# Kernel tuning notes

Measured on AMD Instinct MI355X. Metric: run time of the kernel, lower is better.

Reference implementation:

```python
import jax, jax.numpy as jnp
import numpy as np

EPS = 1e-5  # torch BatchNorm default eps
B, C, T, NOUT, NCLS = 4096, 32, 512, 16, 4


def setup_inputs() -> dict:
    key = jax.random.key(0)
    ks = jax.random.split(key, 12)
    s = lambda k, shape: jax.random.normal(k, shape, jnp.float32) * 0.05
    return {
        "de": jax.random.normal(ks[0], (B, C, T), jnp.float32),
        "adj": jax.random.normal(ks[1], (B, C, C), jnp.float32),  # unused by forward (module recomputes corr)
        "dw_w": s(ks[2], (C, 1, 3)),      # depthwise Conv1d weight [C,1,3]
        "dw_b": s(ks[3], (C,)),
        "pw_w": s(ks[4], (C, C)),          # pointwise 1x1 conv [out,in]
        "pw_b": s(ks[5], (C,)),
        "bn1_g": jnp.ones((C,), jnp.float32),
        "bn1_b": jnp.zeros((C,), jnp.float32),
        "gc_w": s(ks[6], (T, NOUT)),       # GraphConvolution weight
        "fc_w": s(ks[7], (C * NOUT, C)),   # fc62 Linear(512,32)
        "fc_b": s(ks[8], (C,)),
        "bn2_g": jnp.ones((C,), jnp.float32),
        "bn2_b": jnp.zeros((C,), jnp.float32),
        "cls_w": s(ks[9], (C, NCLS)),      # fcclass Linear(32,4)
        "cls_b": s(ks[10], (NCLS,)),
    }


def reference(de, adj, dw_w, dw_b, pw_w, pw_b, bn1_g, bn1_b, gc_w,
              fc_w, fc_b, bn2_g, bn2_b, cls_w, cls_b):
    # --- SeparableConv2d (really 1d): depthwise k=3 -> pointwise 1x1 -> BN -> relu ---
    x = jax.lax.conv_general_dilated(
        de, dw_w, window_strides=(1,), padding=[(1, 1)],
        dimension_numbers=("NCH", "OIH", "NCH"),
        feature_group_count=de.shape[1]) + dw_b[None, :, None]
    x = jnp.einsum("oc,bct->bot", pw_w, x) + pw_b[None, :, None]
    m = x.mean((0, 2), keepdims=True)
    v = x.var((0, 2), keepdims=True)  # biased, as BN normalization uses
    x = (x - m) / jnp.sqrt(v + EPS) * bn1_g[None, :, None] + bn1_b[None, :, None]
    x = jax.nn.relu(x)                       # [B, C, T]

    # --- batched Pearson corrcoef over the time axis (vectorizes the per-sample loop) ---
    xt = x.transpose(0, 2, 1)                # [B, T, C]
    Tn = xt.shape[1]
    f = (Tn - 1) / Tn
    xc = xt - xt.mean(1, keepdims=True)
    num = jnp.einsum("btn,btm->bnm", xc, xc) / Tn   # biased covariance
    var = xt.var(1, ddof=1)                         # torch var default unbiased
    den = jnp.sqrt(var[:, :, None] * var[:, None, :]) * f
    cor = num / den                          # [B, C, C]

    # --- Chebyshev graph convolution (single K term, adj = cor) + relu ---
    g = jnp.einsum("bnm,bmt->bnt", cor, x)   # message passing over channel graph
    g = jax.nn.relu(jnp.einsum("bnt,to->bno", g, gc_w))  # [B, C, 16]

    # --- fc62: Linear -> BN1d -> (dropout: identity) -> sigmoid ---
    h = g.reshape(g.shape[0], -1) @ fc_w + fc_b          # [B, 32]
    m2 = h.mean(0)
    v2 = h.var(0)
    h = (h - m2) / jnp.sqrt(v2 + EPS) * bn2_g + bn2_b
    h = jax.nn.sigmoid(h)

    return h @ cls_w + cls_b                 # [B, 4]
```

## Files before the change

### kernel.cpp

```cpp
#include <hip/hip_runtime.h>
#include <math.h>

#define BB 4096
#define CC 32
#define TT 512
#define NOUTC 16
#define EPSF 1e-5f
#define XS 520


typedef __attribute__((ext_vector_type(16))) float f32x16;
typedef __attribute__((ext_vector_type(4)))  float f32x4;
typedef __attribute__((ext_vector_type(8)))  short short8;
typedef __attribute__((ext_vector_type(8)))  _Float16 half8;
typedef __attribute__((ext_vector_type(4)))  unsigned int u32x4;
typedef __attribute__((ext_vector_type(2)))  unsigned int u32x2;
typedef __attribute__((ext_vector_type(2)))  float vf2;
typedef __attribute__((ext_vector_type(4)))  float vf4;
typedef vf4 __attribute__((aligned(4))) vf4u;
typedef vf2 __attribute__((aligned(4))) vf2u;

__device__ __forceinline__ unsigned short f2b(float f) {
  unsigned int u = __builtin_bit_cast(unsigned int, f);
  return (unsigned short)((u + 0x7FFFu + ((u >> 16) & 1u)) >> 16);
}
__device__ __forceinline__ float blo(unsigned int u) {
  return __builtin_bit_cast(float, u << 16);
}
__device__ __forceinline__ float bhi(unsigned int u) {
  return __builtin_bit_cast(float, u & 0xFFFF0000u);
}
__device__ __forceinline__ unsigned int pk2(float a, float b) {
  return (unsigned int)f2b(a) | ((unsigned int)f2b(b) << 16);
}
__device__ __forceinline__ unsigned short h16(float f) {
  _Float16 h = (_Float16)f;
  return __builtin_bit_cast(unsigned short, h);
}
__device__ __forceinline__ unsigned int h2pk(float a, float b) {
  return (unsigned int)h16(a) | ((unsigned int)h16(b) << 16);
}

__device__ __forceinline__ void conv_cols(const float* __restrict__ deb,
    const float* __restrict__ dw, const float* __restrict__ db_,
    int tid, float* x1A, float* x1B) {
  int t0 = tid * 2;
  int off = (tid == 0) ? 0 : ((tid == 255) ? t0 - 2 : t0 - 1);
#pragma unroll
  for (int c = 0; c < CC; c++) {
    vf4u v = *reinterpret_cast<const vf4u*>(deb + c * TT + off);
    float vm1 = (tid == 0) ? 0.f : ((tid == 255) ? v.y : v.x);
    float v0  = (tid == 0) ? v.x : ((tid == 255) ? v.z : v.y);
    float vp1 = (tid == 0) ? v.y : ((tid == 255) ? v.w : v.z);
    float vp2 = (tid == 0) ? v.z : ((tid == 255) ? 0.f : v.w);
    float w0 = dw[c * 3], w1 = dw[c * 3 + 1], w2 = dw[c * 3 + 2], bc = db_[c];
    x1A[c] = fmaf(w0, vm1, fmaf(w1, v0, fmaf(w2, vp1, bc)));
    x1B[c] = fmaf(w0, v0, fmaf(w1, vp1, fmaf(w2, vp2, bc)));
  }
}

__global__ __launch_bounds__(256, 4) void k1_stats(const float* __restrict__ de,
    const float* __restrict__ dw, const float* __restrict__ db_,
    const float* __restrict__ pw, const float* __restrict__ pwb,
    float* __restrict__ part, unsigned int* __restrict__ x2h, int useWs) {
  __shared__ __align__(16) unsigned short ldsX[258 * 40];
  __shared__ float pbe_s[CC];
  __shared__ float sqb[4][64];

  int tid = threadIdx.x, b = blockIdx.x;
  int lane = tid & 63, w = tid >> 6;
  int m31 = lane & 31, kh = lane >> 5;
  int p = tid >> 7, rp = tid & 127;

  half8 af[3][2];
#pragma unroll
  for (int s = 0; s < 2; s++) {
#pragma unroll
    for (int j = 0; j < 8; j++) {
      int c = s * 16 + kh * 8 + j;
      float pv = pw[m31 * CC + c];
#pragma unroll
      for (int k = 0; k < 3; k++) af[k][s][j] = (_Float16)(pv * dw[c * 3 + k]);
    }
  }
  if (tid < CC) {
    float s = pwb[tid];
#pragma unroll
    for (int c = 0; c < CC; c++) s = fmaf(pw[tid * CC + c], db_[c], s);
    pbe_s[tid] = s;
  }

  const float* deb = de + (size_t)b * CC * TT;
  unsigned int* xw = x2h + (size_t)b * (CC * 256);

  float sA[16], qA[16];
#pragma unroll
  for (int r = 0; r < 16; r++) { sA[r] = 0.f; qA[r] = 0.f; }

#pragma unroll
  for (int h = 0; h < 2; h++) {
    if (h > 0) __syncthreads();
    {
      int t0 = h * 256 + 2 * rp - 1;
      int r0 = 2 * rp;
      int tl = (t0 < 0) ? 0 : t0;
#pragma unroll
      for (int cc = 0; cc < 16; cc += 2) {
        int c = 16 * p + cc;
        vf2 va = *(const vf2u*)(deb + c * TT + tl);
        vf2 vb = *(const vf2u*)(deb + (c + 1) * TT + tl);
        if (t0 < 0) { va.y = va.x; va.x = 0.f; vb.y = vb.x; vb.x = 0.f; }
        *(unsigned int*)&ldsX[r0 * 40 + c] = h2pk(va.x, vb.x);
        *(unsigned int*)&ldsX[(r0 + 1) * 40 + c] = h2pk(va.y, vb.y);
      }
      if (rp >= 126) {
        int r2 = 256 + (rp - 126);
        int t2 = h * 256 + r2 - 1;
#pragma unroll
        for (int cc = 0; cc < 16; cc++) {
          int c = 16 * p + cc;
          float v = (t2 < TT) ? deb[c * TT + t2] : 0.f;
          ldsX[r2 * 40 + c] = h16(v);
        }
      }
    }
    __syncthreads();

#pragma unroll
    for (int i = 0; i < 2; i++) {
      int wt = w * 2 + i;
      f32x16 acc;
#pragma unroll
      for (int r = 0; r < 16; r++) acc[r] = 0.f;
      int rowb = wt * 32 + m31;
#pragma unroll
      for (int k = 0; k < 3; k++) {
#pragma unroll
        for (int s = 0; s < 2; s++) {
          half8 bf = *(const half8*)&ldsX[(rowb + k) * 40 + s * 16 + kh * 8];
          acc = __builtin_amdgcn_mfma_f32_32x32x16_f16(af[k][s], bf, acc, 0, 0, 0);
        }
      }
#pragma unroll
      for (int q4 = 0; q4 < 4; q4++) {
        int ob = 8 * q4 + 4 * kh;
        float v0 = acc[4 * q4 + 0] + pbe_s[ob + 0];
        float v1 = acc[4 * q4 + 1] + pbe_s[ob + 1];
        float v2 = acc[4 * q4 + 2] + pbe_s[ob + 2];
        float v3 = acc[4 * q4 + 3] + pbe_s[ob + 3];
        sA[4 * q4 + 0] += v0; qA[4 * q4 + 0] = fmaf(v0, v0, qA[4 * q4 + 0]);
        sA[4 * q4 + 1] += v1; qA[4 * q4 + 1] = fmaf(v1, v1, qA[4 * q4 + 1]);
        sA[4 * q4 + 2] += v2; qA[4 * q4 + 2] = fmaf(v2, v2, qA[4 * q4 + 2]);
        sA[4 * q4 + 3] += v3; qA[4 * q4 + 3] = fmaf(v3, v3, qA[4 * q4 + 3]);
        if (useWs) {
          u32x2 pr2;
          pr2[0] = pk2(v0, v1);
          pr2[1] = pk2(v2, v3);
          *(u32x2*)(xw + ((((size_t)h * 8 + wt) * 4 + q4) * 2 + kh) * 64 + m31 * 2) = pr2;
        }
      }
    }
  }

#pragma unroll
  for (int r = 0; r < 16; r++) {
    float s = sA[r], q = qA[r];
#pragma unroll
    for (int d = 1; d < 32; d <<= 1) { s += __shfl_xor(s, d); q += __shfl_xor(q, d); }
    sA[r] = s; qA[r] = q;
  }
  if (m31 == 0) {
#pragma unroll
    for (int r = 0; r < 16; r++) {
      int o = (r & 3) + 8 * (r >> 2) + 4 * kh;
      sqb[w][o * 2 + 0] = sA[r];
      sqb[w][o * 2 + 1] = qA[r];
    }
  }
  __syncthreads();
  if (tid < 64) {
    int o = tid >> 1, st = tid & 1;
    float v = sqb[0][tid] + sqb[1][tid] + sqb[2][tid] + sqb[3][tid];
    part[(size_t)(st * 32 + o) * BB + b] = v;
  }
}

__global__ void k2_bn1(const float* __restrict__ part, const float* __restrict__ g,
                       const float* __restrict__ bta, float* __restrict__ ws,
                       const float* __restrict__ gcw, unsigned short* __restrict__ gcf) {
  __shared__ float redS[256], redQ[256];
  int o = blockIdx.x, tid = threadIdx.x;
  {
    int i = o * 256 + tid;
    int e = i & 7, ln = (i >> 3) & 63, j = (i >> 9) & 7, w2 = i >> 12;
    int q = ln >> 4, n16 = ln & 15;
    int t = w2 * 256 + q * 8 + j * 32 + e;
    gcf[i] = f2b(gcw[t * 16 + n16]);
  }
  const float* ps = part + (size_t)o * BB;
  const float* pq = part + (size_t)(CC + o) * BB;
  float s = 0, q = 0;
  for (int i = tid; i < BB; i += 256) { s += ps[i]; q += pq[i]; }
  redS[tid] = s; redQ[tid] = q;
  __syncthreads();
  for (int k = 128; k > 0; k >>= 1) {
    if (tid < k) { redS[tid] += redS[tid + k]; redQ[tid] += redQ[tid + k]; }
    __syncthreads();
  }
  if (tid == 0) {
    float N = (float)BB * (float)TT;
    float mean = redS[0] / N;
    float var = redQ[0] / N - mean * mean;
    float sc = g[o] / sqrtf(var + EPSF);
    ws[o] = sc;
    ws[32 + o] = bta[o] - mean * sc;
  }
}

__global__ __launch_bounds__(256, 3) void k3_main(const float* __restrict__ de,
    const float* __restrict__ dw, const float* __restrict__ db_,
    const float* __restrict__ pw, const float* __restrict__ pwb,
    const float* __restrict__ wsv, const unsigned short* __restrict__ gcf,
    const float* __restrict__ fcw, const float* __restrict__ fcb,
    float* __restrict__ hT, const unsigned int* __restrict__ x2h, int useWs) {
  __shared__ __align__(16) unsigned short x_s[CC * XS];
  __shared__ float gramP[2][CC * CC];
  __shared__ float zP[2][CC * NOUTC];
  __shared__ float red16[CC * 8];
  __shared__ float mu_s[CC], inv_s[CC];
  __shared__ float scsh[64];

  int tid = threadIdx.x, b = blockIdx.x;
  int w = tid >> 6, lane = tid & 63;
  int t0 = tid * 2;

  if (tid < 64) scsh[tid] = wsv[tid];
  __syncthreads();

  if (useWs) {
    const unsigned int* xr = x2h + (size_t)b * (CC * 256);
#pragma unroll
    for (int it = 0; it < 16; it++) {
      int g = it * 256 + tid;
      int m31g = g & 31, khg = (g >> 5) & 1, q4g = (g >> 6) & 3;
      int wtg = (g >> 8) & 7, hg = (g >> 11) & 1;
      u32x2 v = *(const u32x2*)(xr + (size_t)g * 2);
      int ob = 8 * q4g + 4 * khg;
      int t = hg * 256 + wtg * 32 + m31g;
      float f0 = fmaxf(fmaf(blo(v[0]), scsh[ob + 0], scsh[32 + ob + 0]), 0.f);
      float f1 = fmaxf(fmaf(bhi(v[0]), scsh[ob + 1], scsh[32 + ob + 1]), 0.f);
      float f2 = fmaxf(fmaf(blo(v[1]), scsh[ob + 2], scsh[32 + ob + 2]), 0.f);
      float f3 = fmaxf(fmaf(bhi(v[1]), scsh[ob + 3], scsh[32 + ob + 3]), 0.f);
      x_s[(ob + 0) * XS + t] = f2b(f0);
      x_s[(ob + 1) * XS + t] = f2b(f1);
      x_s[(ob + 2) * XS + t] = f2b(f2);
      x_s[(ob + 3) * XS + t] = f2b(f3);
    }
  } else {
    const float* deb = de + (size_t)b * CC * TT;
    float x1A[CC], x1B[CC];
    conv_cols(deb, dw, db_, tid, x1A, x1B);
#pragma unroll
    for (int o = 0; o < CC; o++) {
      float aA = pwb[o], aB = pwb[o];
#pragma unroll
      for (int c = 0; c < CC; c++) { float pv = pw[o * CC + c]; aA = fmaf(pv, x1A[c], aA); aB = fmaf(pv, x1B[c], aB); }
      float sc = scsh[o], sh = scsh[32 + o];
      unsigned short hA = f2b(fmaxf(fmaf(aA, sc, sh), 0.f));
      unsigned short hB = f2b(fmaxf(fmaf(aB, sc, sh), 0.f));
      *(unsigned int*)(&x_s[o * XS + t0]) = (unsigned int)hA | ((unsigned int)hB << 16);
    }
  }
  __syncthreads();

  {
    int c = tid >> 3, j = tid & 7;
    float s = 0.f;
#pragma unroll
    for (int it = 0; it < 8; it++) {
      u32x4 u = *reinterpret_cast<const u32x4*>(&x_s[c * XS + j * 64 + it * 8]);
#pragma unroll
      for (int k = 0; k < 4; k++) s += blo(u[k]) + bhi(u[k]);
    }
    red16[c * 8 + j] = s;
  }

  if (w < 2) {
    int m = lane & 31, kh = lane >> 5;
    f32x16 acc;
#pragma unroll
    for (int r = 0; r < 16; r++) acc[r] = 0.f;
    int kbase = w * 256 + kh * 8;
#pragma unroll
    for (int kk = 0; kk < 256; kk += 16) {
      short8 a = *(const short8*)(&x_s[m * XS + kbase + kk]);
      acc = __builtin_amdgcn_mfma_f32_32x32x16_bf16(a, a, acc, 0, 0, 0);
    }
#pragma unroll
    for (int r = 0; r < 16; r++) {
      int row = (r & 3) + 8 * (r >> 2) + 4 * kh;
      gramP[w][row * CC + m] = acc[r];
    }
  } else {
    int w2 = w - 2;
    int n16 = lane & 15, q = lane >> 4;
    f32x4 ac0, ac1;
#pragma unroll
    for (int r = 0; r < 4; r++) { ac0[r] = 0.f; ac1[r] = 0.f; }
    const unsigned short* gf = gcf + w2 * 4096;
    short8 bfr[8];
#pragma unroll
    for (int j = 0; j < 8; j++) bfr[j] = *(const short8*)(gf + (j * 64 + lane) * 8);
    int kbase = w2 * 256 + q * 8;
#pragma unroll
    for (int j = 0; j < 8; j++) {
      int kk = j * 32;
      short8 af0 = *(const short8*)(&x_s[n16 * XS + kbase + kk]);
      short8 af1 = *(const short8*)(&x_s[(16 + n16) * XS + kbase + kk]);
      ac0 = __builtin_amdgcn_mfma_f32_16x16x32_bf16(af0, bfr[j], ac0, 0, 0, 0);
      ac1 = __builtin_amdgcn_mfma_f32_16x16x32_bf16(af1, bfr[j], ac1, 0, 0, 0);
    }
#pragma unroll
    for (int r = 0; r < 4; r++) {
      int row = q * 4 + r;
      zP[w2][row * NOUTC + n16] = ac0[r];
      zP[w2][(16 + row) * NOUTC + n16] = ac1[r];
    }
  }
  __syncthreads();
  if (tid < CC) {
    float s = 0.f;
#pragma unroll
    for (int j = 0; j < 8; j++) s += red16[tid * 8 + j];
    mu_s[tid] = s;
  }
  __syncthreads();
  float* gram0 = gramP[0];
  float* Zi = zP[0];
  float* g2 = zP[1];
  for (int i = tid; i < CC * CC; i += 256) {
    int n = i >> 5, m = i & 31;
    gram0[i] = gram0[i] + gramP[1][i] - mu_s[n] * mu_s[m] * (1.f / (float)TT);
  }
  for (int i = tid; i < CC * NOUTC; i += 256) Zi[i] = zP[0][i] + zP[1][i];
  __syncthreads();
  if (tid < CC) inv_s[tid] = rsqrtf(gram0[tid * 32 + tid]);
  __syncthreads();
  for (int i = tid; i < CC * NOUTC; i += 256) {
    int n = i >> 4, o = i & 15;
    float s = 0.f;
#pragma unroll
    for (int m = 0; m < CC; m++) s = fmaf(gram0[n * 32 + m] * inv_s[m], Zi[m * NOUTC + o], s);
    g2[i] = fmaxf(s * inv_s[n], 0.f);
  }
  __syncthreads();
  float* red2 = gramP[1];
  {
    int j = tid & 31, ch = tid >> 5;
    float pacc = 0.f;
#pragma unroll
    for (int ii = 0; ii < 64; ii++) {
      int i = ch * 64 + ii;
      pacc = fmaf(g2[i], fcw[i * CC + j], pacc);
    }
    red2[j * 9 + ch] = pacc;
  }
  __syncthreads();
  if (tid < CC) {
    float h = fcb[tid];
#pragma unroll
    for (int ch = 0; ch < 8; ch++) h += red2[tid * 9 + ch];
    hT[(size_t)tid * BB + b] = h;
  }
}

__global__ void k4_bn2(const float* __restrict__ hT, const float* __restrict__ g,
                       const float* __restrict__ bta, float* __restrict__ ws) {
  __shared__ float redS[256], redQ[256];
  int j = blockIdx.x, tid = threadIdx.x;
  const float* row = hT + (size_t)j * BB;
  float s = 0, q = 0;
  for (int i = tid; i < BB; i += 256) { float v = row[i]; s += v; q = fmaf(v, v, q); }
  redS[tid] = s; redQ[tid] = q;
  __syncthreads();
  for (int k = 128; k > 0; k >>= 1) {
    if (tid < k) { redS[tid] += redS[tid + k]; redQ[tid] += redQ[tid + k]; }
    __syncthreads();
  }
  if (tid == 0) {
    float N = (float)BB;
    float mean = redS[0] / N;
    float var = redQ[0] / N - mean * mean;
    float sc = g[j] / sqrtf(var + EPSF);
    ws[64 + j] = sc;
    ws[96 + j] = bta[j] - mean * sc;
  }
}

__global__ void k5_out(const float* __restrict__ hT, const float* __restrict__ ws,
                       const float* __restrict__ clsw, const float* __restrict__ clsb,
                       float* __restrict__ out) {
  __shared__ float hs[CC * 257];
  int b0 = blockIdx.x * 256, tid = threadIdx.x;
  for (int i = tid; i < CC * 256; i += 256) {
    int j = i >> 8, bb = i & 255;
    float v = fmaf(hT[(size_t)j * BB + b0 + bb], ws[64 + j], ws[96 + j]);
    hs[j * 257 + bb] = 1.f / (1.f + expf(-v));
  }
  __syncthreads();
  float o0 = clsb[0], o1 = clsb[1], o2 = clsb[2], o3 = clsb[3];
#pragma unroll
  for (int j = 0; j < CC; j++) {
    float h = hs[j * 257 + tid];
    o0 = fmaf(h, clsw[j * 4 + 0], o0);
    o1 = fmaf(h, clsw[j * 4 + 1], o1);
    o2 = fmaf(h, clsw[j * 4 + 2], o2);
    o3 = fmaf(h, clsw[j * 4 + 3], o3);
  }
  float4* out4 = reinterpret_cast<float4*>(out);
  out4[b0 + tid] = make_float4(o0, o1, o2, o3);
}

extern "C" void kernel_launch(void* const* d_in, const int* in_sizes, int n_in,
                              void* d_out, int out_size, void* d_ws, size_t ws_size,
                              hipStream_t stream) {
  const float* de   = (const float*)d_in[0];
  const float* dw   = (const float*)d_in[2];
  const float* db_  = (const float*)d_in[3];
  const float* pw   = (const float*)d_in[4];
  const float* pwb  = (const float*)d_in[5];
  const float* bn1g = (const float*)d_in[6];
  const float* bn1b = (const float*)d_in[7];
  const float* gcw  = (const float*)d_in[8];
  const float* fcw  = (const float*)d_in[9];
  const float* fcb  = (const float*)d_in[10];
  const float* bn2g = (const float*)d_in[11];
  const float* bn2b = (const float*)d_in[12];
  const float* clsw = (const float*)d_in[13];
  const float* clsb = (const float*)d_in[14];

  float* ws = (float*)d_ws;
  unsigned short* gcf = (unsigned short*)(ws + 128);
  float* hT   = ws + 4224;
  float* part = ws + 135296;
  unsigned int* x2h = (unsigned int*)(ws + 397440);
  float* out  = (float*)d_out;

  size_t need = ((size_t)397440 + 33554432ull) * 4ull;
  int useWs = (ws_size >= need) ? 1 : 0;

  k1_stats<<<BB, 256, 0, stream>>>(de, dw, db_, pw, pwb, part, x2h, useWs);
  k2_bn1<<<CC, 256, 0, stream>>>(part, bn1g, bn1b, ws, gcw, gcf);
  k3_main<<<BB, 256, 0, stream>>>(de, dw, db_, pw, pwb, ws, gcf, fcw, fcb, hT, x2h, useWs);
  k4_bn2<<<CC, 256, 0, stream>>>(hT, bn2g, bn2b, ws);
  k5_out<<<BB / 256, 256, 0, stream>>>(hT, ws, clsw, clsb, out);
}
```

Baseline: 493.4 us.

## Recompute conv+pointwise via MFMA in main kernel instead of workspace round-trip

```diff
diff --git a/kernel.cpp b/kernel.cpp
--- a/kernel.cpp
+++ b/kernel.cpp
@@ -6,7 +6,6 @@
 #define TT 512
 #define NOUTC 16
 #define EPSF 1e-5f
-#define XS 520
 
 
 typedef __attribute__((ext_vector_type(16))) float f32x16;
@@ -14,10 +13,7 @@
 typedef __attribute__((ext_vector_type(8)))  short short8;
 typedef __attribute__((ext_vector_type(8)))  _Float16 half8;
 typedef __attribute__((ext_vector_type(4)))  unsigned int u32x4;
-typedef __attribute__((ext_vector_type(2)))  unsigned int u32x2;
 typedef __attribute__((ext_vector_type(2)))  float vf2;
-typedef __attribute__((ext_vector_type(4)))  float vf4;
-typedef vf4 __attribute__((aligned(4))) vf4u;
 typedef vf2 __attribute__((aligned(4))) vf2u;
 
 __device__ __forceinline__ unsigned short f2b(float f) {
@@ -30,9 +26,6 @@
 __device__ __forceinline__ float bhi(unsigned int u) {
   return __builtin_bit_cast(float, u & 0xFFFF0000u);
 }
-__device__ __forceinline__ unsigned int pk2(float a, float b) {
-  return (unsigned int)f2b(a) | ((unsigned int)f2b(b) << 16);
-}
 __device__ __forceinline__ unsigned short h16(float f) {
   _Float16 h = (_Float16)f;
   return __builtin_bit_cast(unsigned short, h);
@@ -41,28 +34,50 @@
   return (unsigned int)h16(a) | ((unsigned int)h16(b) << 16);
 }
 
-__device__ __forceinline__ void conv_cols(const float* __restrict__ deb,
-    const float* __restrict__ dw, const float* __restrict__ db_,
-    int tid, float* x1A, float* x1B) {
-  int t0 = tid * 2;
-  int off = (tid == 0) ? 0 : ((tid == 255) ? t0 - 2 : t0 - 1);
-#pragma unroll
-  for (int c = 0; c < CC; c++) {
-    vf4u v = *reinterpret_cast<const vf4u*>(deb + c * TT + off);
-    float vm1 = (tid == 0) ? 0.f : ((tid == 255) ? v.y : v.x);
-    float v0  = (tid == 0) ? v.x : ((tid == 255) ? v.z : v.y);
-    float vp1 = (tid == 0) ? v.y : ((tid == 255) ? v.w : v.z);
-    float vp2 = (tid == 0) ? v.z : ((tid == 255) ? 0.f : v.w);
-    float w0 = dw[c * 3], w1 = dw[c * 3 + 1], w2 = dw[c * 3 + 2], bc = db_[c];
-    x1A[c] = fmaf(w0, vm1, fmaf(w1, v0, fmaf(w2, vp1, bc)));
-    x1B[c] = fmaf(w0, v0, fmaf(w1, vp1, fmaf(w2, vp2, bc)));
+__device__ __forceinline__ void stage_xf(unsigned short* xf, const float* __restrict__ deb,
+                                         int h, int p, int rp) {
+  int t0 = h * 256 + 2 * rp - 1;
+  int r0 = 2 * rp;
+  int tl = (t0 < 0) ? 0 : t0;
+#pragma unroll
+  for (int cc = 0; cc < 16; cc += 2) {
+    int c = 16 * p + cc;
+    vf2 va = *(const vf2u*)(deb + c * TT + tl);
+    vf2 vb = *(const vf2u*)(deb + (c + 1) * TT + tl);
+    if (t0 < 0) { va.y = va.x; va.x = 0.f; vb.y = vb.x; vb.x = 0.f; }
+    *(unsigned int*)&xf[r0 * 40 + c] = h2pk(va.x, vb.x);
+    *(unsigned int*)&xf[(r0 + 1) * 40 + c] = h2pk(va.y, vb.y);
+  }
+  if (rp >= 126) {
+    int r2 = 256 + (rp - 126);
+    int t2 = h * 256 + r2 - 1;
+#pragma unroll
+    for (int cc = 0; cc < 16; cc++) {
+      int c = 16 * p + cc;
+      float v = (t2 < TT) ? deb[c * TT + t2] : 0.f;
+      xf[r2 * 40 + c] = h16(v);
+    }
+  }
+}
+
+__device__ __forceinline__ void load_af(half8 af[3][2], const float* __restrict__ pw,
+                                        const float* __restrict__ dw, int m31, int kh) {
+#pragma unroll
+  for (int s = 0; s < 2; s++) {
+#pragma unroll
+    for (int j = 0; j < 8; j++) {
+      int c = s * 16 + kh * 8 + j;
+      float pv = pw[m31 * CC + c];
+#pragma unroll
+      for (int k = 0; k < 3; k++) af[k][s][j] = (_Float16)(pv * dw[c * 3 + k]);
+    }
   }
 }
 
 __global__ __launch_bounds__(256, 4) void k1_stats(const float* __restrict__ de,
     const float* __restrict__ dw, const float* __restrict__ db_,
     const float* __restrict__ pw, const float* __restrict__ pwb,
-    float* __restrict__ part, unsigned int* __restrict__ x2h, int useWs) {
+    float* __restrict__ part) {
   __shared__ __align__(16) unsigned short ldsX[258 * 40];
   __shared__ float pbe_s[CC];
   __shared__ float sqb[4][64];
@@ -73,16 +88,7 @@
   int p = tid >> 7, rp = tid & 127;
 
   half8 af[3][2];
-#pragma unroll
-  for (int s = 0; s < 2; s++) {
-#pragma unroll
-    for (int j = 0; j < 8; j++) {
-      int c = s * 16 + kh * 8 + j;
-      float pv = pw[m31 * CC + c];
-#pragma unroll
-      for (int k = 0; k < 3; k++) af[k][s][j] = (_Float16)(pv * dw[c * 3 + k]);
-    }
-  }
+  load_af(af, pw, dw, m31, kh);
   if (tid < CC) {
     float s = pwb[tid];
 #pragma unroll
@@ -91,8 +97,6 @@
   }
 
   const float* deb = de + (size_t)b * CC * TT;
-  unsigned int* xw = x2h + (size_t)b * (CC * 256);
-
   float sA[16], qA[16];
 #pragma unroll
   for (int r = 0; r < 16; r++) { sA[r] = 0.f; qA[r] = 0.f; }
@@ -100,32 +104,8 @@
 #pragma unroll
   for (int h = 0; h < 2; h++) {
     if (h > 0) __syncthreads();
-    {
-      int t0 = h * 256 + 2 * rp - 1;
-      int r0 = 2 * rp;
-      int tl = (t0 < 0) ? 0 : t0;
-#pragma unroll
-      for (int cc = 0; cc < 16; cc += 2) {
-        int c = 16 * p + cc;
-        vf2 va = *(const vf2u*)(deb + c * TT + tl);
-        vf2 vb = *(const vf2u*)(deb + (c + 1) * TT + tl);
-        if (t0 < 0) { va.y = va.x; va.x = 0.f; vb.y = vb.x; vb.x = 0.f; }
-        *(unsigned int*)&ldsX[r0 * 40 + c] = h2pk(va.x, vb.x);
-        *(unsigned int*)&ldsX[(r0 + 1) * 40 + c] = h2pk(va.y, vb.y);
-      }
-      if (rp >= 126) {
-        int r2 = 256 + (rp - 126);
-        int t2 = h * 256 + r2 - 1;
-#pragma unroll
-        for (int cc = 0; cc < 16; cc++) {
-          int c = 16 * p + cc;
-          float v = (t2 < TT) ? deb[c * TT + t2] : 0.f;
-          ldsX[r2 * 40 + c] = h16(v);
-        }
-      }
-    }
+    stage_xf(ldsX, deb, h, p, rp);
     __syncthreads();
-
 #pragma unroll
     for (int i = 0; i < 2; i++) {
       int wt = w * 2 + i;
@@ -144,19 +124,11 @@
 #pragma unroll
       for (int q4 = 0; q4 < 4; q4++) {
         int ob = 8 * q4 + 4 * kh;
-        float v0 = acc[4 * q4 + 0] + pbe_s[ob + 0];
-        float v1 = acc[4 * q4 + 1] + pbe_s[ob + 1];
-        float v2 = acc[4 * q4 + 2] + pbe_s[ob + 2];
-        float v3 = acc[4 * q4 + 3] + pbe_s[ob + 3];
-        sA[4 * q4 + 0] += v0; qA[4 * q4 + 0] = fmaf(v0, v0, qA[4 * q4 + 0]);
-        sA[4 * q4 + 1] += v1; qA[4 * q4 + 1] = fmaf(v1, v1, qA[4 * q4 + 1]);
-        sA[4 * q4 + 2] += v2; qA[4 * q4 + 2] = fmaf(v2, v2, qA[4 * q4 + 2]);
-        sA[4 * q4 + 3] += v3; qA[4 * q4 + 3] = fmaf(v3, v3, qA[4 * q4 + 3]);
-        if (useWs) {
-          u32x2 pr2;
-          pr2[0] = pk2(v0, v1);
-          pr2[1] = pk2(v2, v3);
-          *(u32x2*)(xw + ((((size_t)h * 8 + wt) * 4 + q4) * 2 + kh) * 64 + m31 * 2) = pr2;
+#pragma unroll
+        for (int j = 0; j < 4; j++) {
+          float v = acc[4 * q4 + j] + pbe_s[ob + j];
+          sA[4 * q4 + j] += v;
+          qA[4 * q4 + j] = fmaf(v, v, qA[4 * q4 + j]);
         }
       }
     }
@@ -222,84 +194,100 @@
     const float* __restrict__ pw, const float* __restrict__ pwb,
     const float* __restrict__ wsv, const unsigned short* __restrict__ gcf,
     const float* __restrict__ fcw, const float* __restrict__ fcb,
-    float* __restrict__ hT, const unsigned int* __restrict__ x2h, int useWs) {
-  __shared__ __align__(16) unsigned short x_s[CC * XS];
-  __shared__ float gramP[2][CC * CC];
-  __shared__ float zP[2][CC * NOUTC];
-  __shared__ float red16[CC * 8];
-  __shared__ float mu_s[CC], inv_s[CC];
-  __shared__ float scsh[64];
+    float* __restrict__ hT) {
+  __shared__ __align__(16) unsigned short x_s[CC * 512];
+  __shared__ __align__(16) unsigned short xfu[10320];
+  __shared__ float sqb[4][CC];
+  __shared__ float scsh2[64];
 
   int tid = threadIdx.x, b = blockIdx.x;
   int w = tid >> 6, lane = tid & 63;
-  int t0 = tid * 2;
-
-  if (tid < 64) scsh[tid] = wsv[tid];
-  __syncthreads();
-
-  if (useWs) {
-    const unsigned int* xr = x2h + (size_t)b * (CC * 256);
-#pragma unroll
-    for (int it = 0; it < 16; it++) {
-      int g = it * 256 + tid;
-      int m31g = g & 31, khg = (g >> 5) & 1, q4g = (g >> 6) & 3;
-      int wtg = (g >> 8) & 7, hg = (g >> 11) & 1;
-      u32x2 v = *(const u32x2*)(xr + (size_t)g * 2);
-      int ob = 8 * q4g + 4 * khg;
-      int t = hg * 256 + wtg * 32 + m31g;
-      float f0 = fmaxf(fmaf(blo(v[0]), scsh[ob + 0], scsh[32 + ob + 0]), 0.f);
-      float f1 = fmaxf(fmaf(bhi(v[0]), scsh[ob + 1], scsh[32 + ob + 1]), 0.f);
-      float f2 = fmaxf(fmaf(blo(v[1]), scsh[ob + 2], scsh[32 + ob + 2]), 0.f);
-      float f3 = fmaxf(fmaf(bhi(v[1]), scsh[ob + 3], scsh[32 + ob + 3]), 0.f);
-      x_s[(ob + 0) * XS + t] = f2b(f0);
-      x_s[(ob + 1) * XS + t] = f2b(f1);
-      x_s[(ob + 2) * XS + t] = f2b(f2);
-      x_s[(ob + 3) * XS + t] = f2b(f3);
-    }
-  } else {
-    const float* deb = de + (size_t)b * CC * TT;
-    float x1A[CC], x1B[CC];
-    conv_cols(deb, dw, db_, tid, x1A, x1B);
-#pragma unroll
-    for (int o = 0; o < CC; o++) {
-      float aA = pwb[o], aB = pwb[o];
-#pragma unroll
-      for (int c = 0; c < CC; c++) { float pv = pw[o * CC + c]; aA = fmaf(pv, x1A[c], aA); aB = fmaf(pv, x1B[c], aB); }
-      float sc = scsh[o], sh = scsh[32 + o];
-      unsigned short hA = f2b(fmaxf(fmaf(aA, sc, sh), 0.f));
-      unsigned short hB = f2b(fmaxf(fmaf(aB, sc, sh), 0.f));
-      *(unsigned int*)(&x_s[o * XS + t0]) = (unsigned int)hA | ((unsigned int)hB << 16);
-    }
-  }
-  __syncthreads();
-
-  {
-    int c = tid >> 3, j = tid & 7;
-    float s = 0.f;
-#pragma unroll
-    for (int it = 0; it < 8; it++) {
-      u32x4 u = *reinterpret_cast<const u32x4*>(&x_s[c * XS + j * 64 + it * 8]);
-#pragma unroll
-      for (int k = 0; k < 4; k++) s += blo(u[k]) + bhi(u[k]);
-    }
-    red16[c * 8 + j] = s;
-  }
+  int m31 = lane & 31, kh = lane >> 5;
+  int p = tid >> 7, rp = tid & 127;
+
+  if (tid < CC) {
+    float pb = pwb[tid];
+#pragma unroll
+    for (int c = 0; c < CC; c++) pb = fmaf(pw[tid * CC + c], db_[c], pb);
+    float sc = wsv[tid];
+    scsh2[tid] = sc;
+    scsh2[32 + tid] = fmaf(sc, pb, wsv[32 + tid]);
+  }
+
+  half8 af[3][2];
+  load_af(af, pw, dw, m31, kh);
+
+  const float* deb = de + (size_t)b * CC * TT;
+  float muA[16];
+#pragma unroll
+  for (int r = 0; r < 16; r++) muA[r] = 0.f;
+
+#pragma unroll
+  for (int h = 0; h < 2; h++) {
+    if (h > 0) __syncthreads();
+    stage_xf(xfu, deb, h, p, rp);
+    __syncthreads();
+#pragma unroll
+    for (int i = 0; i < 2; i++) {
+      int wt = w * 2 + i;
+      f32x16 acc;
+#pragma unroll
+      for (int r = 0; r < 16; r++) acc[r] = 0.f;
+      int rowb = wt * 32 + m31;
+#pragma unroll
+      for (int k = 0; k < 3; k++) {
+#pragma unroll
+        for (int s = 0; s < 2; s++) {
+          half8 bf = *(const half8*)&xfu[(rowb + k) * 40 + s * 16 + kh * 8];
+          acc = __builtin_amdgcn_mfma_f32_32x32x16_f16(af[k][s], bf, acc, 0, 0, 0);
+        }
+      }
+      int tglob = h * 256 + wt * 32 + m31;
+#pragma unroll
+      for (int q4 = 0; q4 < 4; q4++) {
+        int ob = 8 * q4 + 4 * kh;
+#pragma unroll
+        for (int j = 0; j < 4; j++) {
+          int o = ob + j;
+          float f = fmaxf(fmaf(acc[4 * q4 + j], scsh2[o], scsh2[32 + o]), 0.f);
+          muA[4 * q4 + j] += f;
+          x_s[(o * 512 + tglob) ^ ((o & 7) << 3)] = f2b(f);
+        }
+      }
+    }
+  }
+
+#pragma unroll
+  for (int r = 0; r < 16; r++) {
+    float s = muA[r];
+#pragma unroll
+    for (int d = 1; d < 32; d <<= 1) s += __shfl_xor(s, d);
+    muA[r] = s;
+  }
+  if (m31 == 0) {
+#pragma unroll
+    for (int r = 0; r < 16; r++) sqb[w][(r & 3) + 8 * (r >> 2) + 4 * kh] = muA[r];
+  }
+  __syncthreads();
+
+  float* gramP = (float*)xfu;
+  float* zP = gramP + 2048;
 
   if (w < 2) {
-    int m = lane & 31, kh = lane >> 5;
+    int m = lane & 31, kh2 = lane >> 5;
     f32x16 acc;
 #pragma unroll
     for (int r = 0; r < 16; r++) acc[r] = 0.f;
-    int kbase = w * 256 + kh * 8;
+    int kbase = w * 256 + kh2 * 8;
 #pragma unroll
     for (int kk = 0; kk < 256; kk += 16) {
-      short8 a = *(const short8*)(&x_s[m * XS + kbase + kk]);
+      short8 a = *(const short8*)(&x_s[(m * 512 + kbase + kk) ^ ((m & 7) << 3)]);
       acc = __builtin_amdgcn_mfma_f32_32x32x16_bf16(a, a, acc, 0, 0, 0);
     }
 #pragma unroll
     for (int r = 0; r < 16; r++) {
-      int row = (r & 3) + 8 * (r >> 2) + 4 * kh;
-      gramP[w][row * CC + m] = acc[r];
+      int row = (r & 3) + 8 * (r >> 2) + 4 * kh2;
+      gramP[w * 1024 + row * CC + m] = acc[r];
     }
   } else {
     int w2 = w - 2;
@@ -315,46 +303,45 @@
 #pragma unroll
     for (int j = 0; j < 8; j++) {
       int kk = j * 32;
-      short8 af0 = *(const short8*)(&x_s[n16 * XS + kbase + kk]);
-      short8 af1 = *(const short8*)(&x_s[(16 + n16) * XS + kbase + kk]);
+      short8 af0 = *(const short8*)(&x_s[(n16 * 512 + kbase + kk) ^ ((n16 & 7) << 3)]);
+      short8 af1 = *(const short8*)(&x_s[((16 + n16) * 512 + kbase + kk) ^ ((n16 & 7) << 3)]);
       ac0 = __builtin_amdgcn_mfma_f32_16x16x32_bf16(af0, bfr[j], ac0, 0, 0, 0);
       ac1 = __builtin_amdgcn_mfma_f32_16x16x32_bf16(af1, bfr[j], ac1, 0, 0, 0);
     }
 #pragma unroll
     for (int r = 0; r < 4; r++) {
       int row = q * 4 + r;
-      zP[w2][row * NOUTC + n16] = ac0[r];
-      zP[w2][(16 + row) * NOUTC + n16] = ac1[r];
-    }
-  }
-  __syncthreads();
+      zP[w2 * 512 + row * NOUTC + n16] = ac0[r];
+      zP[w2 * 512 + (16 + row) * NOUTC + n16] = ac1[r];
+    }
+  }
+  __syncthreads();
+
   if (tid < CC) {
-    float s = 0.f;
-#pragma unroll
-    for (int j = 0; j < 8; j++) s += red16[tid * 8 + j];
-    mu_s[tid] = s;
-  }
-  __syncthreads();
-  float* gram0 = gramP[0];
-  float* Zi = zP[0];
-  float* g2 = zP[1];
+    float m4 = sqb[0][tid] + sqb[1][tid] + sqb[2][tid] + sqb[3][tid];
+    sqb[0][tid] = m4;
+  }
+  __syncthreads();
+  float* gram0 = gramP;
+  float* Zi = zP;
+  float* g2 = zP + 512;
   for (int i = tid; i < CC * CC; i += 256) {
     int n = i >> 5, m = i & 31;
-    gram0[i] = gram0[i] + gramP[1][i] - mu_s[n] * mu_s[m] * (1.f / (float)TT);
-  }
-  for (int i = tid; i < CC * NOUTC; i += 256) Zi[i] = zP[0][i] + zP[1][i];
-  __syncthreads();
-  if (tid < CC) inv_s[tid] = rsqrtf(gram0[tid * 32 + tid]);
+    gram0[i] = gram0[i] + gramP[1024 + i] - sqb[0][n] * sqb[0][m] * (1.f / (float)TT);
+  }
+  for (int i = tid; i < CC * NOUTC; i += 256) Zi[i] = zP[i] + zP[512 + i];
+  __syncthreads();
+  if (tid < CC) sqb[1][tid] = rsqrtf(gram0[tid * 32 + tid]);
   __syncthreads();
   for (int i = tid; i < CC * NOUTC; i += 256) {
     int n = i >> 4, o = i & 15;
     float s = 0.f;
 #pragma unroll
-    for (int m = 0; m < CC; m++) s = fmaf(gram0[n * 32 + m] * inv_s[m], Zi[m * NOUTC + o], s);
-    g2[i] = fmaxf(s * inv_s[n], 0.f);
-  }
-  __syncthreads();
-  float* red2 = gramP[1];
+    for (int m = 0; m < CC; m++) s = fmaf(gram0[n * 32 + m] * sqb[1][m], Zi[m * NOUTC + o], s);
+    g2[i] = fmaxf(s * sqb[1][n], 0.f);
+  }
+  __syncthreads();
+  float* red2 = gramP + 1024;
   {
     int j = tid & 31, ch = tid >> 5;
     float pacc = 0.f;
@@ -443,15 +430,11 @@
   unsigned short* gcf = (unsigned short*)(ws + 128);
   float* hT   = ws + 4224;
   float* part = ws + 135296;
-  unsigned int* x2h = (unsigned int*)(ws + 397440);
   float* out  = (float*)d_out;
 
-  size_t need = ((size_t)397440 + 33554432ull) * 4ull;
-  int useWs = (ws_size >= need) ? 1 : 0;
-
-  k1_stats<<<BB, 256, 0, stream>>>(de, dw, db_, pw, pwb, part, x2h, useWs);
+  k1_stats<<<BB, 256, 0, stream>>>(de, dw, db_, pw, pwb, part);
   k2_bn1<<<CC, 256, 0, stream>>>(part, bn1g, bn1b, ws, gcw, gcf);
-  k3_main<<<BB, 256, 0, stream>>>(de, dw, db_, pw, pwb, ws, gcf, fcw, fcb, hT, x2h, useWs);
+  k3_main<<<BB, 256, 0, stream>>>(de, dw, db_, pw, pwb, ws, gcf, fcw, fcb, hT);
   k4_bn2<<<CC, 256, 0, stream>>>(hT, bn2g, bn2b, ws);
   k5_out<<<BB / 256, 256, 0, stream>>>(hT, ws, clsw, clsb, out);
 }
```

New measurement: 655.1 us. 32.8% more time.

## Issue all input loads upfront into registers and double the LDS staging buffer

Applied to the files above, without the earlier changes.

```diff
diff --git a/kernel.cpp b/kernel.cpp
--- a/kernel.cpp
+++ b/kernel.cpp
@@ -59,11 +59,49 @@
   }
 }
 
-__global__ __launch_bounds__(256, 4) void k1_stats(const float* __restrict__ de,
+__device__ __forceinline__ void load_af(half8 af[3][2], const float* __restrict__ pw,
+                                        const float* __restrict__ dw, int m31, int kh) {
+#pragma unroll
+  for (int s = 0; s < 2; s++) {
+#pragma unroll
+    for (int j = 0; j < 8; j++) {
+      int c = s * 16 + kh * 8 + j;
+      float pv = pw[m31 * CC + c];
+#pragma unroll
+      for (int k = 0; k < 3; k++) af[k][s][j] = (_Float16)(pv * dw[c * 3 + k]);
+    }
+  }
+}
+
+__device__ __forceinline__ void load_half(const float* __restrict__ deb, int h, int p, int rp,
+                                          vf2 r[16]) {
+  int t0 = h * 256 + 2 * rp - 1;
+  int tl = (t0 < 0) ? 0 : t0;
+#pragma unroll
+  for (int cc = 0; cc < 16; cc++) {
+    int c = 16 * p + cc;
+    r[cc] = *(const vf2u*)(deb + c * TT + tl);
+  }
+}
+
+__device__ __forceinline__ void write_half(unsigned short* xf, vf2 r[16], int h, int p, int rp) {
+  int t0 = h * 256 + 2 * rp - 1;
+  int r0 = 2 * rp;
+#pragma unroll
+  for (int cc = 0; cc < 16; cc += 2) {
+    int c = 16 * p + cc;
+    vf2 va = r[cc], vb = r[cc + 1];
+    if (t0 < 0) { va.y = va.x; va.x = 0.f; vb.y = vb.x; vb.x = 0.f; }
+    *(unsigned int*)&xf[r0 * 40 + c] = h2pk(va.x, vb.x);
+    *(unsigned int*)&xf[(r0 + 1) * 40 + c] = h2pk(va.y, vb.y);
+  }
+}
+
+__global__ __launch_bounds__(256, 3) void k1_stats(const float* __restrict__ de,
     const float* __restrict__ dw, const float* __restrict__ db_,
     const float* __restrict__ pw, const float* __restrict__ pwb,
     float* __restrict__ part, unsigned int* __restrict__ x2h, int useWs) {
-  __shared__ __align__(16) unsigned short ldsX[258 * 40];
+  __shared__ __align__(16) unsigned short ldsX[2][258 * 40];
   __shared__ float pbe_s[CC];
   __shared__ float sqb[4][64];
 
@@ -72,17 +110,18 @@
   int m31 = lane & 31, kh = lane >> 5;
   int p = tid >> 7, rp = tid & 127;
 
+  const float* deb = de + (size_t)b * CC * TT;
+
+  vf2 rA[16], rB[16];
+  load_half(deb, 0, p, rp, rA);
+  load_half(deb, 1, p, rp, rB);
+  int eh = tid >> 6, ej = (tid >> 5) & 1, ec = tid & 31;
+  int et = eh * 256 + 255 + ej;
+  float ev = 0.f;
+  if (tid < 128 && et < TT) ev = deb[ec * TT + et];
+
   half8 af[3][2];
-#pragma unroll
-  for (int s = 0; s < 2; s++) {
-#pragma unroll
-    for (int j = 0; j < 8; j++) {
-      int c = s * 16 + kh * 8 + j;
-      float pv = pw[m31 * CC + c];
-#pragma unroll
-      for (int k = 0; k < 3; k++) af[k][s][j] = (_Float16)(pv * dw[c * 3 + k]);
-    }
-  }
+  load_af(af, pw, dw, m31, kh);
   if (tid < CC) {
     float s = pwb[tid];
 #pragma unroll
@@ -90,42 +129,19 @@
     pbe_s[tid] = s;
   }
 
-  const float* deb = de + (size_t)b * CC * TT;
+  write_half(ldsX[0], rA, 0, p, rp);
+  write_half(ldsX[1], rB, 1, p, rp);
+  if (tid < 128) ldsX[eh][(256 + ej) * 40 + ec] = h16(ev);
+  __syncthreads();
+
   unsigned int* xw = x2h + (size_t)b * (CC * 256);
-
   float sA[16], qA[16];
 #pragma unroll
   for (int r = 0; r < 16; r++) { sA[r] = 0.f; qA[r] = 0.f; }
 
 #pragma unroll
   for (int h = 0; h < 2; h++) {
-    if (h > 0) __syncthreads();
-    {
-      int t0 = h * 256 + 2 * rp - 1;
-      int r0 = 2 * rp;
-      int tl = (t0 < 0) ? 0 : t0;
-#pragma unroll
-      for (int cc = 0; cc < 16; cc += 2) {
-        int c = 16 * p + cc;
-        vf2 va = *(const vf2u*)(deb + c * TT + tl);
-        vf2 vb = *(const vf2u*)(deb + (c + 1) * TT + tl);
-        if (t0 < 0) { va.y = va.x; va.x = 0.f; vb.y = vb.x; vb.x = 0.f; }
-        *(unsigned int*)&ldsX[r0 * 40 + c] = h2pk(va.x, vb.x);
-        *(unsigned int*)&ldsX[(r0 + 1) * 40 + c] = h2pk(va.y, vb.y);
-      }
-      if (rp >= 126) {
-        int r2 = 256 + (rp - 126);
-        int t2 = h * 256 + r2 - 1;
-#pragma unroll
-        for (int cc = 0; cc < 16; cc++) {
-          int c = 16 * p + cc;
-          float v = (t2 < TT) ? deb[c * TT + t2] : 0.f;
-          ldsX[r2 * 40 + c] = h16(v);
-        }
-      }
-    }
-    __syncthreads();
-
+    const unsigned short* xf = ldsX[h];
 #pragma unroll
     for (int i = 0; i < 2; i++) {
       int wt = w * 2 + i;
@@ -137,7 +153,7 @@
       for (int k = 0; k < 3; k++) {
 #pragma unroll
         for (int s = 0; s < 2; s++) {
-          half8 bf = *(const half8*)&ldsX[(rowb + k) * 40 + s * 16 + kh * 8];
+          half8 bf = *(const half8*)&xf[(rowb + k) * 40 + s * 16 + kh * 8];
           acc = __builtin_amdgcn_mfma_f32_32x32x16_f16(af[k][s], bf, acc, 0, 0, 0);
         }
       }
```

After: 472.7 us. 1.04x faster.

## Split k1 into two blocks per sample and widen k3 workspace loads

Applied to the files above, without the earlier changes.

```diff
diff --git a/kernel.cpp b/kernel.cpp
--- a/kernel.cpp
+++ b/kernel.cpp
@@ -2,6 +2,7 @@
 #include <math.h>
 
 #define BB 4096
+#define BB2 8192
 #define CC 32
 #define TT 512
 #define NOUTC 16
@@ -59,6 +60,20 @@
   }
 }
 
+__device__ __forceinline__ void load_af(half8 af[3][2], const float* __restrict__ pw,
+                                        const float* __restrict__ dw, int m31, int kh) {
+#pragma unroll
+  for (int s = 0; s < 2; s++) {
+#pragma unroll
+    for (int j = 0; j < 8; j++) {
+      int c = s * 16 + kh * 8 + j;
+      float pv = pw[m31 * CC + c];
+#pragma unroll
+      for (int k = 0; k < 3; k++) af[k][s][j] = (_Float16)(pv * dw[c * 3 + k]);
+    }
+  }
+}
+
 __global__ __launch_bounds__(256, 4) void k1_stats(const float* __restrict__ de,
     const float* __restrict__ dw, const float* __restrict__ db_,
     const float* __restrict__ pw, const float* __restrict__ pwb,
@@ -67,22 +82,31 @@
   __shared__ float pbe_s[CC];
   __shared__ float sqb[4][64];
 
-  int tid = threadIdx.x, b = blockIdx.x;
+  int tid = threadIdx.x, bh = blockIdx.x;
+  int b = bh >> 1, h = bh & 1;
   int lane = tid & 63, w = tid >> 6;
   int m31 = lane & 31, kh = lane >> 5;
   int p = tid >> 7, rp = tid & 127;
 
+  const float* deb = de + (size_t)b * CC * TT;
+
+  vf2 rA[16];
+  {
+    int t0 = h * 256 + 2 * rp - 1;
+    int tl = (t0 < 0) ? 0 : t0;
+#pragma unroll
+    for (int cc = 0; cc < 16; cc++) {
+      int c = 16 * p + cc;
+      rA[cc] = *(const vf2u*)(deb + c * TT + tl);
+    }
+  }
+  int ej = (tid >> 5) & 1, ec = tid & 31;
+  int et = h * 256 + 255 + ej;
+  float ev = 0.f;
+  if (tid < 64 && et < TT) ev = deb[ec * TT + et];
+
   half8 af[3][2];
-#pragma unroll
-  for (int s = 0; s < 2; s++) {
-#pragma unroll
-    for (int j = 0; j < 8; j++) {
-      int c = s * 16 + kh * 8 + j;
-      float pv = pw[m31 * CC + c];
-#pragma unroll
-      for (int k = 0; k < 3; k++) af[k][s][j] = (_Float16)(pv * dw[c * 3 + k]);
-    }
-  }
+  load_af(af, pw, dw, m31, kh);
   if (tid < CC) {
     float s = pwb[tid];
 #pragma unroll
@@ -90,74 +114,57 @@
     pbe_s[tid] = s;
   }
 
-  const float* deb = de + (size_t)b * CC * TT;
+  {
+    int t0 = h * 256 + 2 * rp - 1;
+    int r0 = 2 * rp;
+#pragma unroll
+    for (int cc = 0; cc < 16; cc += 2) {
+      int c = 16 * p + cc;
+      vf2 va = rA[cc], vb = rA[cc + 1];
+      if (t0 < 0) { va.y = va.x; va.x = 0.f; vb.y = vb.x; vb.x = 0.f; }
+      *(unsigned int*)&ldsX[r0 * 40 + c] = h2pk(va.x, vb.x);
+      *(unsigned int*)&ldsX[(r0 + 1) * 40 + c] = h2pk(va.y, vb.y);
+    }
+  }
+  if (tid < 64) ldsX[(256 + ej) * 40 + ec] = h16(ev);
+  __syncthreads();
+
   unsigned int* xw = x2h + (size_t)b * (CC * 256);
-
   float sA[16], qA[16];
 #pragma unroll
   for (int r = 0; r < 16; r++) { sA[r] = 0.f; qA[r] = 0.f; }
 
 #pragma unroll
-  for (int h = 0; h < 2; h++) {
-    if (h > 0) __syncthreads();
-    {
-      int t0 = h * 256 + 2 * rp - 1;
-      int r0 = 2 * rp;
-      int tl = (t0 < 0) ? 0 : t0;
-#pragma unroll
-      for (int cc = 0; cc < 16; cc += 2) {
-        int c = 16 * p + cc;
-        vf2 va = *(const vf2u*)(deb + c * TT + tl);
-        vf2 vb = *(const vf2u*)(deb + (c + 1) * TT + tl);
-        if (t0 < 0) { va.y = va.x; va.x = 0.f; vb.y = vb.x; vb.x = 0.f; }
-        *(unsigned int*)&ldsX[r0 * 40 + c] = h2pk(va.x, vb.x);
-        *(unsigned int*)&ldsX[(r0 + 1) * 40 + c] = h2pk(va.y, vb.y);
+  for (int i = 0; i < 2; i++) {
+    int wt = w * 2 + i;
+    f32x16 acc;
+#pragma unroll
+    for (int r = 0; r < 16; r++) acc[r] = 0.f;
+    int rowb = wt * 32 + m31;
+#pragma unroll
+    for (int k = 0; k < 3; k++) {
+#pragma unroll
+      for (int s = 0; s < 2; s++) {
+        half8 bf = *(const half8*)&ldsX[(rowb + k) * 40 + s * 16 + kh * 8];
+        acc = __builtin_amdgcn_mfma_f32_32x32x16_f16(af[k][s], bf, acc, 0, 0, 0);
       }
-      if (rp >= 126) {
-        int r2 = 256 + (rp - 126);
-        int t2 = h * 256 + r2 - 1;
-#pragma unroll
-        for (int cc = 0; cc < 16; cc++) {
-          int c = 16 * p + cc;
-          float v = (t2 < TT) ? deb[c * TT + t2] : 0.f;
-          ldsX[r2 * 40 + c] = h16(v);
-        }
-      }
-    }
-    __syncthreads();
-
-#pragma unroll
-    for (int i = 0; i < 2; i++) {
-      int wt = w * 2 + i;
-      f32x16 acc;
-#pragma unroll
-      for (int r = 0; r < 16; r++) acc[r] = 0.f;
-      int rowb = wt * 32 + m31;
-#pragma unroll
-      for (int k = 0; k < 3; k++) {
-#pragma unroll
-        for (int s = 0; s < 2; s++) {
-          half8 bf = *(const half8*)&ldsX[(rowb + k) * 40 + s * 16 + kh * 8];
-          acc = __builtin_amdgcn_mfma_f32_32x32x16_f16(af[k][s], bf, acc, 0, 0, 0);
-        }
-      }
-#pragma unroll
-      for (int q4 = 0; q4 < 4; q4++) {
-        int ob = 8 * q4 + 4 * kh;
-        float v0 = acc[4 * q4 + 0] + pbe_s[ob + 0];
-        float v1 = acc[4 * q4 + 1] + pbe_s[ob + 1];
-        float v2 = acc[4 * q4 + 2] + pbe_s[ob + 2];
-        float v3 = acc[4 * q4 + 3] + pbe_s[ob + 3];
-        sA[4 * q4 + 0] += v0; qA[4 * q4 + 0] = fmaf(v0, v0, qA[4 * q4 + 0]);
-        sA[4 * q4 + 1] += v1; qA[4 * q4 + 1] = fmaf(v1, v1, qA[4 * q4 + 1]);
-        sA[4 * q4 + 2] += v2; qA[4 * q4 + 2] = fmaf(v2, v2, qA[4 * q4 + 2]);
-        sA[4 * q4 + 3] += v3; qA[4 * q4 + 3] = fmaf(v3, v3, qA[4 * q4 + 3]);
-        if (useWs) {
-          u32x2 pr2;
-          pr2[0] = pk2(v0, v1);
-          pr2[1] = pk2(v2, v3);
-          *(u32x2*)(xw + ((((size_t)h * 8 + wt) * 4 + q4) * 2 + kh) * 64 + m31 * 2) = pr2;
-        }
+    }
+#pragma unroll
+    for (int q4 = 0; q4 < 4; q4++) {
+      int ob = 8 * q4 + 4 * kh;
+      float v0 = acc[4 * q4 + 0] + pbe_s[ob + 0];
+      float v1 = acc[4 * q4 + 1] + pbe_s[ob + 1];
+      float v2 = acc[4 * q4 + 2] + pbe_s[ob + 2];
+      float v3 = acc[4 * q4 + 3] + pbe_s[ob + 3];
+      sA[4 * q4 + 0] += v0; qA[4 * q4 + 0] = fmaf(v0, v0, qA[4 * q4 + 0]);
+      sA[4 * q4 + 1] += v1; qA[4 * q4 + 1] = fmaf(v1, v1, qA[4 * q4 + 1]);
+      sA[4 * q4 + 2] += v2; qA[4 * q4 + 2] = fmaf(v2, v2, qA[4 * q4 + 2]);
+      sA[4 * q4 + 3] += v3; qA[4 * q4 + 3] = fmaf(v3, v3, qA[4 * q4 + 3]);
+      if (useWs) {
+        u32x2 pr2;
+        pr2[0] = pk2(v0, v1);
+        pr2[1] = pk2(v2, v3);
+        *(u32x2*)(xw + ((((size_t)h * 8 + wt) * 4 + q4) * 2 + kh) * 64 + m31 * 2) = pr2;
       }
     }
   }
@@ -181,7 +188,7 @@
   if (tid < 64) {
     int o = tid >> 1, st = tid & 1;
     float v = sqb[0][tid] + sqb[1][tid] + sqb[2][tid] + sqb[3][tid];
-    part[(size_t)(st * 32 + o) * BB + b] = v;
+    part[(size_t)(st * 32 + o) * BB2 + bh] = v;
   }
 }
 
@@ -197,10 +204,10 @@
     int t = w2 * 256 + q * 8 + j * 32 + e;
     gcf[i] = f2b(gcw[t * 16 + n16]);
   }
-  const float* ps = part + (size_t)o * BB;
-  const float* pq = part + (size_t)(CC + o) * BB;
+  const float* ps = part + (size_t)o * BB2;
+  const float* pq = part + (size_t)(CC + o) * BB2;
   float s = 0, q = 0;
-  for (int i = tid; i < BB; i += 256) { s += ps[i]; q += pq[i]; }
+  for (int i = tid; i < BB2; i += 256) { s += ps[i]; q += pq[i]; }
   redS[tid] = s; redQ[tid] = q;
   __syncthreads();
   for (int k = 128; k > 0; k >>= 1) {
@@ -238,23 +245,29 @@
   __syncthreads();
 
   if (useWs) {
-    const unsigned int* xr = x2h + (size_t)b * (CC * 256);
-#pragma unroll
-    for (int it = 0; it < 16; it++) {
+    const u32x4* xr4 = (const u32x4*)(x2h + (size_t)b * (CC * 256));
+#pragma unroll
+    for (int it = 0; it < 8; it++) {
       int g = it * 256 + tid;
-      int m31g = g & 31, khg = (g >> 5) & 1, q4g = (g >> 6) & 3;
-      int wtg = (g >> 8) & 7, hg = (g >> 11) & 1;
-      u32x2 v = *(const u32x2*)(xr + (size_t)g * 2);
+      u32x4 v = xr4[g];
+      int pg = g * 2;
+      int m31g = pg & 31;
+      int khg = (pg >> 5) & 1, q4g = (pg >> 6) & 3;
+      int wtg = (pg >> 8) & 7, hg = (pg >> 11) & 1;
       int ob = 8 * q4g + 4 * khg;
       int t = hg * 256 + wtg * 32 + m31g;
-      float f0 = fmaxf(fmaf(blo(v[0]), scsh[ob + 0], scsh[32 + ob + 0]), 0.f);
-      float f1 = fmaxf(fmaf(bhi(v[0]), scsh[ob + 1], scsh[32 + ob + 1]), 0.f);
-      float f2 = fmaxf(fmaf(blo(v[1]), scsh[ob + 2], scsh[32 + ob + 2]), 0.f);
-      float f3 = fmaxf(fmaf(bhi(v[1]), scsh[ob + 3], scsh[32 + ob + 3]), 0.f);
-      x_s[(ob + 0) * XS + t] = f2b(f0);
-      x_s[(ob + 1) * XS + t] = f2b(f1);
-      x_s[(ob + 2) * XS + t] = f2b(f2);
-      x_s[(ob + 3) * XS + t] = f2b(f3);
+      float sc0 = scsh[ob + 0], sh0 = scsh[32 + ob + 0];
+      float sc1 = scsh[ob + 1], sh1 = scsh[32 + ob + 1];
+      float sc2 = scsh[ob + 2], sh2 = scsh[32 + ob + 2];
+      float sc3 = scsh[ob + 3], sh3 = scsh[32 + ob + 3];
+      float a0 = fmaxf(fmaf(blo(v[0]), sc0, sh0), 0.f), b0 = fmaxf(fmaf(blo(v[2]), sc0, sh0), 0.f);
+      float a1 = fmaxf(fmaf(bhi(v[0]), sc1, sh1), 0.f), b1 = fmaxf(fmaf(bhi(v[2]), sc1, sh1), 0.f);
+      float a2 = fmaxf(fmaf(blo(v[1]), sc2, sh2), 0.f), b2 = fmaxf(fmaf(blo(v[3]), sc2, sh2), 0.f);
+      float a3 = fmaxf(fmaf(bhi(v[1]), sc3, sh3), 0.f), b3 = fmaxf(fmaf(bhi(v[3]), sc3, sh3), 0.f);
+      *(unsigned int*)&x_s[(ob + 0) * XS + t] = pk2(a0, b0);
+      *(unsigned int*)&x_s[(ob + 1) * XS + t] = pk2(a1, b1);
+      *(unsigned int*)&x_s[(ob + 2) * XS + t] = pk2(a2, b2);
+      *(unsigned int*)&x_s[(ob + 3) * XS + t] = pk2(a3, b3);
     }
   } else {
     const float* deb = de + (size_t)b * CC * TT;
@@ -443,13 +456,13 @@
   unsigned short* gcf = (unsigned short*)(ws + 128);
   float* hT   = ws + 4224;
   float* part = ws + 135296;
-  unsigned int* x2h = (unsigned int*)(ws + 397440);
+  unsigned int* x2h = (unsigned int*)(ws + 659584);
   float* out  = (float*)d_out;
 
-  size_t need = ((size_t)397440 + 33554432ull) * 4ull;
+  size_t need = ((size_t)659584 + 33554432ull) * 4ull;
   int useWs = (ws_size >= need) ? 1 : 0;
 
-  k1_stats<<<BB, 256, 0, stream>>>(de, dw, db_, pw, pwb, part, x2h, useWs);
+  k1_stats<<<BB2, 256, 0, stream>>>(de, dw, db_, pw, pwb, part, x2h, useWs);
   k2_bn1<<<CC, 256, 0, stream>>>(part, bn1g, bn1b, ws, gcw, gcf);
   k3_main<<<BB, 256, 0, stream>>>(de, dw, db_, pw, pwb, ws, gcf, fcw, fcb, hT, x2h, useWs);
   k4_bn2<<<CC, 256, 0, stream>>>(hT, bn2g, bn2b, ws);
```

Result: no change. 490.5 us (-0.6%).
